# Performance work log

Hardware: AMD Instinct MI355X
Metric: run time of the kernel (lower is better)

Reference implementation:

```python
import jax, jax.numpy as jnp
import numpy as np

B, C, H, W = 4, 64, 64, 64

def setup_inputs() -> dict:
    key = jax.random.key(0)
    ks = jax.random.split(key, 7)
    s = 1.0 / np.sqrt(C)
    return {
        "x": jax.random.normal(ks[0], (B, C, H, W), dtype=jnp.float32),
        "Wq": jax.random.normal(ks[1], (C, C), dtype=jnp.float32) * s,
        "bq": jax.random.normal(ks[2], (C,), dtype=jnp.float32) * s,
        "Wk": jax.random.normal(ks[3], (C, C), dtype=jnp.float32) * s,
        "bk": jax.random.normal(ks[4], (C,), dtype=jnp.float32) * s,
        "Wv": jax.random.normal(ks[5], (C, C), dtype=jnp.float32) * s,
        "bv": jax.random.normal(ks[6], (C,), dtype=jnp.float32) * s,
    }

def reference(x, Wq, bq, Wk, bk, Wv, bv):
    b, c, h, w = x.shape
    n = h * w
    xf = x.reshape(b, c, n)                                   # (B,C,N)
    # 1x1 convs == per-pixel linear maps over channels
    q = jnp.einsum('oc,bcn->bon', Wq, xf) + bq[None, :, None]  # (B,C,N)
    k = jnp.einsum('oc,bcn->bon', Wk, xf) + bk[None, :, None]  # (B,C,N)
    v = jnp.einsum('oc,bcn->bon', Wv, xf) + bv[None, :, None]  # (B,C,N)
    # energy = Q^T K : (B,N,N); note: no 1/sqrt(C) scaling in the original
    energy = jnp.einsum('bcn,bcm->bnm', q, k)
    attention = jax.nn.softmax(energy, axis=-1)
    # out = V @ attention^T : out[:, :, i] = sum_j V[:, :, j] * attention[i, j]
    out = jnp.einsum('bcm,bnm->bcn', v, attention)
    return out.reshape(b, c, h, w)
```

## Files before the change

### kernel.cpp

```cpp
#include <hip/hip_runtime.h>
#include <math.h>

#define T_N 4096
#define T_C 64
#define T_B 4
#define NSLICE 8
#define TILES_PER_SLICE (64 / NSLICE)
#define LOG2E 1.44269504088896f

typedef __attribute__((ext_vector_type(8))) _Float16 f16x8;
typedef __attribute__((ext_vector_type(4))) short s16x4;
typedef __attribute__((ext_vector_type(4))) float f32x4;

#define MFMA_BF16(a, b, c) __builtin_amdgcn_mfma_f32_16x16x16bf16_1k(a, b, c, 0, 0, 0)

__device__ inline unsigned short f2h(float f) {
    union { _Float16 h; unsigned short s; } u; u.h = (_Float16)f; return u.s;
}
__device__ inline float h2f(unsigned short s) {
    union { unsigned short s; _Float16 h; } u; u.s = s; return (float)u.h;
}
__device__ inline unsigned short f2bf(float f) {
    union { float f; unsigned u; } x; x.f = f;
    return (unsigned short)((x.u + 0x7FFFu + ((x.u >> 16) & 1u)) >> 16);
}
__device__ inline float fexp2(float x) { return __builtin_amdgcn_exp2f(x); }

#define DMA16(g, l) __builtin_amdgcn_global_load_lds(                         \
    (const __attribute__((address_space(1))) void*)(g),                       \
    (__attribute__((address_space(3))) void*)(l), 16, 0, 0)

__global__ __launch_bounds__(256) void qkv_kernel(
    const float* __restrict__ x,
    const float* __restrict__ Wq, const float* __restrict__ bq,
    const float* __restrict__ Wk, const float* __restrict__ bk,
    const float* __restrict__ Wv, const float* __restrict__ bv,
    unsigned short* __restrict__ qt, unsigned short* __restrict__ kt,
    unsigned short* __restrict__ vb)
{
    __shared__ __align__(16) unsigned short xsh[32 * 72];
    __shared__ __align__(16) unsigned short xsl[32 * 72];
    __shared__ __align__(16) unsigned short wf[3][64 * 72];

    const int tid = threadIdx.x;
    const int n0  = blockIdx.x * 32;
    const int b   = blockIdx.y;
    const float* xb = x + (size_t)b * T_C * T_N;

    const float* Ws[3] = {Wq, Wk, Wv};
    #pragma unroll
    for (int p = 0; p < 3; ++p) {
        const float sc = (p == 0) ? LOG2E : 1.0f;
        for (int i = tid; i < 1024; i += 256) {
            const int o = i >> 4, c4 = (i & 15) * 4;
            const float4 w4 = ((const float4*)Ws[p])[i];
            f16x8 wh;
            wh[0] = (_Float16)(w4.x * sc); wh[1] = (_Float16)(w4.y * sc);
            wh[2] = (_Float16)(w4.z * sc); wh[3] = (_Float16)(w4.w * sc);
            *(ushort4*)&wf[p][o * 72 + c4] = *(ushort4*)&wh;
        }
    }
    for (int i = tid; i < 512; i += 256) {
        const int c = i >> 3, nj4 = (i & 7) * 4;
        const float4 xv = *(const float4*)&xb[c * T_N + n0 + nj4];
        const float xa[4] = {xv.x, xv.y, xv.z, xv.w};
        #pragma unroll
        for (int j = 0; j < 4; ++j) {
            const unsigned short h = f2h(xa[j]);
            xsh[(nj4 + j) * 72 + c] = h;
            xsl[(nj4 + j) * 72 + c] = f2h(xa[j] - h2f(h));
        }
    }
    __syncthreads();

    const int wv_  = tid >> 6;
    const int lane = tid & 63;
    const int quad = lane >> 4;
    const int col  = lane & 15;
    const int pst  = (wv_ & 1) * 16;
    const int oh   = (wv_ >> 1) * 2;
    const size_t bN = (size_t)b * T_N;

    f16x8 xh[2], xl[2];
    #pragma unroll
    for (int s = 0; s < 2; ++s) {
        xh[s] = *(const f16x8*)&xsh[(pst + col) * 72 + s * 32 + quad * 8];
        xl[s] = *(const f16x8*)&xsl[(pst + col) * 72 + s * 32 + quad * 8];
    }
    __syncthreads();

    const float* biases[3] = {bq, bk, bv};
    for (int p = 0; p < 3; ++p) {
        #pragma unroll
        for (int oo = 0; oo < 2; ++oo) {
            const int osub = oh + oo;
            f32x4 acc = (f32x4){0.f, 0.f, 0.f, 0.f};
            #pragma unroll
            for (int s = 0; s < 2; ++s) {
                const f16x8 wfr =
                    *(const f16x8*)&wf[p][(osub * 16 + col) * 72 + s * 32 + quad * 8];
                acc = __builtin_amdgcn_mfma_f32_16x16x32_f16(xh[s], wfr, acc, 0, 0, 0);
                acc = __builtin_amdgcn_mfma_f32_16x16x32_f16(xl[s], wfr, acc, 0, 0, 0);
            }
            const float bb = biases[p][osub * 16 + col] * ((p == 0) ? LOG2E : 1.0f);
            if (p < 2) {
                #pragma unroll
                for (int r = 0; r < 4; ++r)
                    xsh[(pst + quad * 4 + r) * 72 + osub * 16 + col] = f2h(acc[r] + bb);
            } else {
                union { ushort4 v; unsigned short s[4]; } hv;
                #pragma unroll
                for (int r = 0; r < 4; ++r) hv.s[r] = f2bf(acc[r] + bb);
                *(ushort4*)&xsh[(osub * 16 + col) * 36 + pst + quad * 4] = hv.v;
            }
        }
        __syncthreads();
        if (p < 2) {
            const int pix = tid >> 3, c8 = (tid & 7) * 8;
            unsigned short* dst = (p == 0) ? qt : kt;
            *(f16x8*)&dst[(bN + n0 + pix) * 64 + c8] = *(const f16x8*)&xsh[pix * 72 + c8];
            __syncthreads();
        } else {
            const int o = tid >> 2, p8 = (tid & 3) * 8;
            *(f16x8*)&vb[((size_t)(b * 64 + o)) * T_N + n0 + p8] =
                *(const f16x8*)&xsh[o * 36 + p8];
        }
    }
}

__global__ __launch_bounds__(256, 2) void attn_kernel(
    const unsigned short* __restrict__ qt,
    const unsigned short* __restrict__ kt, const unsigned short* __restrict__ vb,
    unsigned short* __restrict__ o_part, float* __restrict__ lp)
{
    __shared__ __align__(16) unsigned short ks[2][64 * 64];
    __shared__ __align__(16) unsigned short vs[2][64 * 64];

    const int tid   = threadIdx.x;
    const int bid   = blockIdx.x;
    const int slice = bid & 7;
    const int n0    = ((bid >> 3) & 15) * 256;
    const int b     = bid >> 7;
    const int wv_   = tid >> 6;
    const int lane  = tid & 63;
    const int quad  = lane >> 4;
    const int col   = lane & 15;

    const size_t bN = (size_t)b * T_N;
    const int q0 = n0 + wv_ * 64 + col;

    f16x8 qh[4][2];
    #pragma unroll
    for (int g = 0; g < 4; ++g)
        #pragma unroll
        for (int s = 0; s < 2; ++s)
            qh[g][s] = *(const f16x8*)&qt[(bN + q0 + g * 16) * 64 + s * 32 + quad * 8];

    const int row  = tid >> 3, cc = tid & 7;
    const int scc8 = (cc ^ (row & 7)) * 8;
    const int ldst = row * 64 + cc * 8;

    const int mbase = slice * TILES_PER_SLICE * 64;
    const unsigned short* kg_base = &kt[(bN + mbase + row) * 64 + scc8];
    const unsigned short* vg_base = &vb[((size_t)(b * 64 + row)) * T_N + mbase + scc8];

    DMA16(kg_base,                    &ks[0][ldst]);
    DMA16(kg_base + 32 * 64,          &ks[0][32 * 64 + ldst]);
    DMA16(vg_base,                    &vs[0][ldst]);
    DMA16(vg_base + (size_t)32 * T_N, &vs[0][32 * 64 + ldst]);

    f32x4 O[4][4];
    float lsum[4];
    #pragma unroll
    for (int g = 0; g < 4; ++g) {
        lsum[g] = 0.f;
        #pragma unroll
        for (int t = 0; t < 4; ++t)
            O[g][t] = (f32x4){0.f, 0.f, 0.f, 0.f};
    }

    for (int it = 0; it < TILES_PER_SLICE; ++it) {
        __syncthreads();
        const int cur = it & 1;

        {
            const int itn = (it < TILES_PER_SLICE - 1) ? it + 1 : it;
            const unsigned short* kgn = kg_base + itn * (64 * 64);
            const unsigned short* vgn = vg_base + itn * 64;
            const int nb = cur ^ 1;
            DMA16(kgn,                    &ks[nb][ldst]);
            DMA16(kgn + 32 * 64,          &ks[nb][32 * 64 + ldst]);
            DMA16(vgn,                    &vs[nb][ldst]);
            DMA16(vgn + (size_t)32 * T_N, &vs[nb][32 * 64 + ldst]);
        }
        const unsigned short* ksb = ks[cur];
        const unsigned short* vsb = vs[cur];

        f32x4 acc[4][4];
        #pragma unroll
        for (int g = 0; g < 4; ++g)
            #pragma unroll
            for (int t = 0; t < 4; ++t)
                acc[g][t] = (f32x4){0.f, 0.f, 0.f, 0.f};
        __builtin_amdgcn_s_setprio(1);
        #pragma unroll
        for (int s = 0; s < 2; ++s) {
            #pragma unroll
            for (int t = 0; t < 4; ++t) {
                const f16x8 kf = *(const f16x8*)
                    &ksb[(t * 16 + col) * 64 + (((s * 4 + quad) ^ (col & 7)) * 8)];
                #pragma unroll
                for (int g = 0; g < 4; ++g)
                    acc[g][t] = __builtin_amdgcn_mfma_f32_16x16x32_f16(
                        kf, qh[g][s], acc[g][t], 0, 0, 0);
            }
        }
        __builtin_amdgcn_s_setprio(0);

        s16x4 pf[4][4];
        #pragma unroll
        for (int g = 0; g < 4; ++g) {
            #pragma unroll
            for (int t = 0; t < 4; ++t) {
                float pv[4];
                union { unsigned short s[4]; s16x4 v; } pk;
                #pragma unroll
                for (int r = 0; r < 4; ++r) {
                    pv[r] = fexp2(acc[g][t][r]);
                    union { float f; unsigned u; } x; x.f = pv[r];
                    pk.s[r] = (unsigned short)(x.u >> 16);
                }
                pf[g][t] = pk.v;
                lsum[g] += (pv[0] + pv[1]) + (pv[2] + pv[3]);
            }
        }

        __builtin_amdgcn_s_setprio(1);
        #pragma unroll
        for (int tc = 0; tc < 4; ++tc) {
            #pragma unroll
            for (int t = 0; t < 4; ++t) {
                const s16x4 vf = *(const s16x4*)
                    &vsb[(tc * 16 + col) * 64 +
                         (((2 * t + (quad >> 1)) ^ (col & 7)) * 8) + (quad & 1) * 4];
                #pragma unroll
                for (int g = 0; g < 4; ++g)
                    O[g][tc] = MFMA_BF16(vf, pf[g][t], O[g][tc]);
            }
        }
        __builtin_amdgcn_s_setprio(0);
    }

    float inv[4], lfull[4];
    #pragma unroll
    for (int g = 0; g < 4; ++g) {
        float s = lsum[g];
        s += __shfl_xor(s, 16);
        s += __shfl_xor(s, 32);
        lfull[g] = s;
        inv[g] = 1.0f / s;
    }

    const size_t srow = (size_t)(slice * T_B + b) * 64;
    #pragma unroll
    for (int tc = 0; tc < 4; ++tc) {
        #pragma unroll
        for (int r = 0; r < 4; ++r) {
            const size_t crow = (srow + tc * 16 + quad * 4 + r) * T_N;
            #pragma unroll
            for (int g = 0; g < 4; ++g)
                o_part[crow + q0 + g * 16] = f2h(O[g][tc][r] * inv[g]);
        }
    }
    if (quad == 0) {
        const size_t off = (size_t)(slice * T_B + b) * T_N;
        #pragma unroll
        for (int g = 0; g < 4; ++g)
            lp[off + q0 + g * 16] = lfull[g];
    }
}

__global__ __launch_bounds__(256) void combine_kernel(
    const unsigned short* __restrict__ o_part,
    const float* __restrict__ lp, float* __restrict__ out)
{
    __shared__ float wn[NSLICE][32];

    const int tid = threadIdx.x;
    const int n0  = blockIdx.x * 32;
    const int b   = blockIdx.y;

    if (tid < 32) {
        float l_s[NSLICE], L = 0.f;
        #pragma unroll
        for (int s = 0; s < NSLICE; ++s) {
            l_s[s] = lp[(size_t)(s * T_B + b) * T_N + n0 + tid];
            L += l_s[s];
        }
        const float inv = 1.f / L;
        #pragma unroll
        for (int s = 0; s < NSLICE; ++s) wn[s][tid] = l_s[s] * inv;
    }
    __syncthreads();

    for (int t = tid; t < 512; t += 256) {
        const int c = t >> 3, g = t & 7;
        float4 acc = make_float4(0.f, 0.f, 0.f, 0.f);
        #pragma unroll
        for (int s = 0; s < NSLICE; ++s) {
            const ushort4 o4 = *(const ushort4*)
                &o_part[((size_t)((s * T_B + b) * 64 + c)) * T_N + n0 + g * 4];
            acc.x = fmaf(h2f(o4.x), wn[s][g * 4 + 0], acc.x);
            acc.y = fmaf(h2f(o4.y), wn[s][g * 4 + 1], acc.y);
            acc.z = fmaf(h2f(o4.z), wn[s][g * 4 + 2], acc.z);
            acc.w = fmaf(h2f(o4.w), wn[s][g * 4 + 3], acc.w);
        }
        *(float4*)&out[((size_t)(b * 64 + c)) * T_N + n0 + g * 4] = acc;
    }
}

extern "C" void kernel_launch(void* const* d_in, const int* in_sizes, int n_in,
                              void* d_out, int out_size, void* d_ws, size_t ws_size,
                              hipStream_t stream) {
    const float* x  = (const float*)d_in[0];
    const float* Wq = (const float*)d_in[1];
    const float* bq = (const float*)d_in[2];
    const float* Wk = (const float*)d_in[3];
    const float* bk = (const float*)d_in[4];
    const float* Wv = (const float*)d_in[5];
    const float* bv = (const float*)d_in[6];
    float* outp = (float*)d_out;

    const size_t elems = (size_t)T_B * T_N * T_C;
    unsigned short* qtp    = (unsigned short*)d_ws;
    unsigned short* ktp    = qtp + elems;
    unsigned short* vbuf   = ktp + elems;
    unsigned short* o_part = vbuf + elems;
    float* lp = (float*)(o_part + (size_t)NSLICE * elems);

    qkv_kernel<<<dim3(T_N / 32, T_B), 256, 0, stream>>>(
        x, Wq, bq, Wk, bk, Wv, bv, qtp, ktp, vbuf);
    attn_kernel<<<dim3(T_N / 256 * NSLICE * T_B), 256, 0, stream>>>(
        qtp, ktp, vbuf, o_part, lp);
    combine_kernel<<<dim3(T_N / 32, T_B), 256, 0, stream>>>(
        o_part, lp, outp);
}
```

Baseline: 110.0 us.

## Fuse slice combine into attention kernel via last-block atomic counter

Removes the separate combine kernel launch. Each attention block increments a per-(q-tile,batch) counter after writing its partial output, and the last slice block to finish performs the weighted reduction over slices and writes the final output. The counter is zeroed in the QKV kernel. This saves a launch and its gap, but concentrates the combine work on fewer blocks at the tail of the attention kernel.

Measured after the change: 211.8 us. 92.5% more time.

```diff
diff --git a/kernel.cpp b/kernel.cpp
--- a/kernel.cpp
+++ b/kernel.cpp
@@ -36,7 +36,7 @@
     const float* __restrict__ Wk, const float* __restrict__ bk,
     const float* __restrict__ Wv, const float* __restrict__ bv,
     unsigned short* __restrict__ qt, unsigned short* __restrict__ kt,
-    unsigned short* __restrict__ vb)
+    unsigned short* __restrict__ vb, int* __restrict__ cnt)
 {
     __shared__ __align__(16) unsigned short xsh[32 * 72];
     __shared__ __align__(16) unsigned short xsl[32 * 72];
@@ -46,6 +46,9 @@
     const int n0  = blockIdx.x * 32;
     const int b   = blockIdx.y;
     const float* xb = x + (size_t)b * T_C * T_N;
+
+    if ((blockIdx.x & 7) == 0 && tid == 0)
+        cnt[(blockIdx.x >> 3) * T_B + b] = 0;
 
     const float* Ws[3] = {Wq, Wk, Wv};
     #pragma unroll
@@ -131,15 +134,18 @@
 __global__ __launch_bounds__(256, 2) void attn_kernel(
     const unsigned short* __restrict__ qt,
     const unsigned short* __restrict__ kt, const unsigned short* __restrict__ vb,
-    unsigned short* __restrict__ o_part, float* __restrict__ lp)
+    unsigned short* __restrict__ o_part, float* __restrict__ lp,
+    float* __restrict__ out, int* __restrict__ cnt)
 {
     __shared__ __align__(16) unsigned short ks[2][64 * 64];
     __shared__ __align__(16) unsigned short vs[2][64 * 64];
+    __shared__ int s_old;
 
     const int tid   = threadIdx.x;
     const int bid   = blockIdx.x;
     const int slice = bid & 7;
-    const int n0    = ((bid >> 3) & 15) * 256;
+    const int qx    = (bid >> 3) & 15;
+    const int n0    = qx * 256;
     const int b     = bid >> 7;
     const int wv_   = tid >> 6;
     const int lane  = tid & 63;
@@ -278,44 +284,41 @@
         for (int g = 0; g < 4; ++g)
             lp[off + q0 + g * 16] = lfull[g];
     }
-}
-
-__global__ __launch_bounds__(256) void combine_kernel(
-    const unsigned short* __restrict__ o_part,
-    const float* __restrict__ lp, float* __restrict__ out)
-{
-    __shared__ float wn[NSLICE][32];
-
-    const int tid = threadIdx.x;
-    const int n0  = blockIdx.x * 32;
-    const int b   = blockIdx.y;
-
-    if (tid < 32) {
+
+    __threadfence();
+    if (tid == 0) s_old = atomicAdd(&cnt[qx * T_B + b], 1);
+    __syncthreads();
+    if (s_old != NSLICE - 1) return;
+    __threadfence();
+
+    float* wn = (float*)&ks[0][0];
+    {
+        const int q = n0 + tid;
         float l_s[NSLICE], L = 0.f;
         #pragma unroll
         for (int s = 0; s < NSLICE; ++s) {
-            l_s[s] = lp[(size_t)(s * T_B + b) * T_N + n0 + tid];
+            l_s[s] = lp[(size_t)(s * T_B + b) * T_N + q];
             L += l_s[s];
         }
-        const float inv = 1.f / L;
-        #pragma unroll
-        for (int s = 0; s < NSLICE; ++s) wn[s][tid] = l_s[s] * inv;
+        const float invL = 1.f / L;
+        #pragma unroll
+        for (int s = 0; s < NSLICE; ++s) wn[s * 256 + tid] = l_s[s] * invL;
     }
     __syncthreads();
 
-    for (int t = tid; t < 512; t += 256) {
-        const int c = t >> 3, g = t & 7;
+    for (int i = tid; i < 64 * 64; i += 256) {
+        const int c = i >> 6, j = i & 63;
         float4 acc = make_float4(0.f, 0.f, 0.f, 0.f);
         #pragma unroll
         for (int s = 0; s < NSLICE; ++s) {
             const ushort4 o4 = *(const ushort4*)
-                &o_part[((size_t)((s * T_B + b) * 64 + c)) * T_N + n0 + g * 4];
-            acc.x = fmaf(h2f(o4.x), wn[s][g * 4 + 0], acc.x);
-            acc.y = fmaf(h2f(o4.y), wn[s][g * 4 + 1], acc.y);
-            acc.z = fmaf(h2f(o4.z), wn[s][g * 4 + 2], acc.z);
-            acc.w = fmaf(h2f(o4.w), wn[s][g * 4 + 3], acc.w);
-        }
-        *(float4*)&out[((size_t)(b * 64 + c)) * T_N + n0 + g * 4] = acc;
+                &o_part[((size_t)((s * T_B + b) * 64 + c)) * T_N + n0 + j * 4];
+            acc.x = fmaf(h2f(o4.x), wn[s * 256 + j * 4 + 0], acc.x);
+            acc.y = fmaf(h2f(o4.y), wn[s * 256 + j * 4 + 1], acc.y);
+            acc.z = fmaf(h2f(o4.z), wn[s * 256 + j * 4 + 2], acc.z);
+            acc.w = fmaf(h2f(o4.w), wn[s * 256 + j * 4 + 3], acc.w);
+        }
+        *(float4*)&out[((size_t)(b * 64 + c)) * T_N + n0 + j * 4] = acc;
     }
 }
 
@@ -337,11 +340,10 @@
     unsigned short* vbuf   = ktp + elems;
     unsigned short* o_part = vbuf + elems;
     float* lp = (float*)(o_part + (size_t)NSLICE * elems);
+    int*   cnt = (int*)(lp + (size_t)NSLICE * T_B * T_N);
 
     qkv_kernel<<<dim3(T_N / 32, T_B), 256, 0, stream>>>(
-        x, Wq, bq, Wk, bk, Wv, bv, qtp, ktp, vbuf);
+        x, Wq, bq, Wk, bk, Wv, bv, qtp, ktp, vbuf, cnt);
     attn_kernel<<<dim3(T_N / 256 * NSLICE * T_B), 256, 0, stream>>>(
-        qtp, ktp, vbuf, o_part, lp);
-    combine_kernel<<<dim3(T_N / 32, T_B), 256, 0, stream>>>(
-        o_part, lp, outp);
-}
+        qtp, ktp, vbuf, o_part, lp, outp, cnt);
+}
```
